# Kernel optimization log

Hardware: AMD Instinct MI355X
Metric: run time of the kernel (lower is better)

## Reference

```python
import jax, jax.numpy as jnp
import numpy as np

# per-item cutpoint counts (from np.unique(item_positions, return_counts=True))
NUM_CUTS = np.array([4, 5, 6, 7] * 4)  # 16 items
N_ITEMS = len(NUM_CUTS)
MAX_CP = int(NUM_CUTS.max())  # 7
CP = jnp.asarray(NUM_CUTS)  # [I]
CUT_MASK = jnp.arange(MAX_CP)[None, :] < CP[:, None]  # [I, MAX_CP] valid cutpoints
EPS = 1e-8

B, D_IN, H1, H2 = 65536, 512, 1024, 512


def setup_inputs() -> dict:
    key = jax.random.key(0)
    ks = jax.random.split(key, 10)
    x = jax.random.normal(ks[0], (B, D_IN), dtype=jnp.float32)
    data = jax.random.randint(ks[1], (B, N_ITEMS), 0, 4, dtype=jnp.int64 if jax.config.jax_enable_x64 else jnp.int32)
    W1 = jax.random.normal(ks[2], (D_IN, H1), dtype=jnp.float32) / np.sqrt(D_IN)
    b1 = jnp.zeros((H1,), jnp.float32)
    W2 = jax.random.normal(ks[3], (H1, H2), dtype=jnp.float32) / np.sqrt(H1)
    b2 = jnp.zeros((H2,), jnp.float32)
    Wf = jax.random.normal(ks[4], (H2, N_ITEMS), dtype=jnp.float32) / np.sqrt(H2)
    bf = jnp.zeros((N_ITEMS,), jnp.float32)
    # ragged per-item cutpoint heads padded to MAX_CP (masked in reference)
    Wk = jax.random.normal(ks[5], (N_ITEMS, H2, MAX_CP), dtype=jnp.float32) / np.sqrt(H2)
    bk = jnp.zeros((N_ITEMS, MAX_CP), jnp.float32)
    return {"x": x, "data": data, "W1": W1, "b1": b1, "W2": W2, "b2": b2,
            "Wf": Wf, "bf": bf, "Wk": Wk, "bk": bk}


def reference(x, data, W1, b1, W2, b2, Wf, bf, Wk, bk):
    # trunk MLP: Linear -> ReLU, twice
    h = jax.nn.relu(x @ W1 + b1)
    h = jax.nn.relu(h @ W2 + b2)  # [B, H2]
    f_x = h @ Wf + bf  # [B, I]
    # batched ragged per-item cutpoint heads (padded GEMM + mask)
    cut = jnp.einsum('bh,ihc->bic', h, Wk) + bk  # [B, I, MAX_CP]
    e = jnp.where(CUT_MASK[None], jnp.clip(jnp.exp(cut), EPS, None), 0.0)
    cum = jnp.cumsum(e, axis=-1)  # monotone cutpoints; pads contribute 0
    cum_probs = jnp.clip(jax.nn.sigmoid(cum - f_x[:, :, None]), EPS, 1.0 - EPS)
    # category probs: [cum0, diffs..., 1 - cum_last], ragged lengths cp_i + 1
    diff = jnp.concatenate([cum_probs[..., :1], cum_probs[..., 1:] - cum_probs[..., :-1]], axis=-1)
    last_cum = cum_probs[:, jnp.arange(N_ITEMS), CP - 1]  # [B, I]
    diff_pad = jnp.pad(diff, ((0, 0), (0, 0), (0, 1)))  # [B, I, MAX_CP+1]
    cat = jnp.arange(MAX_CP + 1)[None, None, :]
    probs = jnp.where(cat < CP[None, :, None], diff_pad,
                      jnp.where(cat == CP[None, :, None], (1.0 - last_cum)[:, :, None], 1.0))
    probs = jnp.clip(probs, EPS, 1.0 - EPS)  # [B, I, MAX_CP+1]
    # NLL: gather observed category per (respondent, item)
    gathered = jnp.take_along_axis(probs, data[:, :, None].astype(jnp.int32), axis=2)[..., 0]
    rec_loss = -jnp.log(gathered).mean(axis=0).sum()
    return rec_loss, probs
```

## Files before the change

### kernel.cpp

```cpp
#include <hip/hip_runtime.h>
#include <cmath>

#define EPSV 1e-8f

typedef __bf16 bf16_t;
typedef __bf16 bf16x8 __attribute__((ext_vector_type(8)));
typedef __bf16 bf16x4 __attribute__((ext_vector_type(4)));
typedef float f32x4 __attribute__((ext_vector_type(4)));

__device__ __forceinline__ void gload16(const void* g, void* l) {
    __builtin_amdgcn_global_load_lds(
        (const __attribute__((address_space(1))) void*)g,
        (__attribute__((address_space(3))) void*)l, 16, 0, 0);
}

__device__ __forceinline__ void qmap(int q, int& row, int& u) {
    int prow = q >> 3;
    int v = (q & 7) ^ (prow & 7);
    row = (prow << 1) | (v >> 2);
    u = v & 3;
}
__device__ __forceinline__ int lds_elem(int row, int u) {
    int prow = row >> 1;
    int v = ((row & 1) << 2) | u;
    return prow * 64 + ((v ^ (prow & 7)) << 3);
}

template<bool RELU>
__global__ __launch_bounds__(512, 2) void gemm256(
    const bf16_t* __restrict__ A, const bf16_t* __restrict__ BT,
    const float* __restrict__ bias, bf16_t* __restrict__ C,
    int N, int K, int nbx)
{
    __shared__ bf16_t sm[2][2][2][8192];

    const int t    = threadIdx.x;
    const int lane = t & 63;
    const int w    = t >> 6;
    const int wr   = w >> 2;
    const int wc   = w & 3;
    const int r16  = lane & 15;
    const int u16  = lane >> 4;

    const int nwg = gridDim.x;
    int bid = blockIdx.x;
    int swz = ((nwg & 7) == 0) ? ((bid & 7) * (nwg >> 3) + (bid >> 3)) : bid;
    const int bx = swz % nbx, by = swz / nbx;
    const int m0 = by << 8, n0 = bx << 8;

    int r0, u0, r1, u1;
    qmap(t, r0, u0);
    qmap(t + 512, r1, u1);
    const bf16_t* gA0 = A  + (size_t)(m0 + r0) * K + (u0 << 3);
    const bf16_t* gA1 = A  + (size_t)(m0 + r1) * K + (u1 << 3);
    const bf16_t* gB0 = BT + (size_t)(n0 + r0) * K + (u0 << 3);
    const bf16_t* gB1 = BT + (size_t)(n0 + r1) * K + (u1 << 3);

    auto STAGE = [&](const bf16_t* g0, const bf16_t* g1, bf16_t* sl, int koff) {
        gload16(g0 + koff, sl + (w << 9));
        gload16(g1 + koff, sl + 4096 + (w << 9));
    };

    int aoff[8], boff[4];
#pragma unroll
    for (int i = 0; i < 8; ++i) aoff[i] = lds_elem((wr << 7) + (i << 4) + r16, u16);
#pragma unroll
    for (int j = 0; j < 4; ++j) boff[j] = lds_elem((wc << 6) + (j << 4) + r16, u16);

    f32x4 acc[8][4];
#pragma unroll
    for (int i = 0; i < 8; ++i)
#pragma unroll
        for (int j = 0; j < 4; ++j) acc[i][j] = (f32x4){0.f, 0.f, 0.f, 0.f};

    const int NT = K >> 6;

    STAGE(gA0, gA1, &sm[0][0][0][0], 0);
    STAGE(gB0, gB1, &sm[0][1][0][0], 0);
    STAGE(gA0, gA1, &sm[0][0][1][0], 32);
    STAGE(gB0, gB1, &sm[0][1][1][0], 32);
    STAGE(gA0, gA1, &sm[1][0][0][0], 64);
    STAGE(gB0, gB1, &sm[1][1][0][0], 64);
    asm volatile("s_waitcnt vmcnt(8)" ::: "memory");
    __builtin_amdgcn_s_barrier();

    for (int kt = 0; kt < NT; ++kt) {
        const int c  = kt & 1;
        const int c1 = c ^ 1;
        const bool s12 = (kt + 1) < NT;
        const bool s34 = (kt + 2) < NT;
        const int k12 = ((kt + 1) << 6) + 32;
        const int k34 = (kt + 2) << 6;
        const bf16_t* sA0 = &sm[c][0][0][0];
        const bf16_t* sA1 = &sm[c][0][1][0];
        const bf16_t* sB0 = &sm[c][1][0][0];
        const bf16_t* sB1 = &sm[c][1][1][0];

        bf16x8 af[4], bfr[4];

#pragma unroll
        for (int j = 0; j < 4; ++j) bfr[j] = *(const bf16x8*)(sB0 + boff[j]);
#pragma unroll
        for (int i = 0; i < 4; ++i) af[i] = *(const bf16x8*)(sA0 + aoff[i]);
        if (s12) STAGE(gA0, gA1, &sm[c1][0][1][0], k12);
        __builtin_amdgcn_s_barrier();
        __builtin_amdgcn_s_setprio(1);
#pragma unroll
        for (int i = 0; i < 4; ++i)
#pragma unroll
            for (int j = 0; j < 4; ++j)
                acc[i][j] = __builtin_amdgcn_mfma_f32_16x16x32_bf16(bfr[j], af[i], acc[i][j], 0, 0, 0);
        __builtin_amdgcn_s_setprio(0);
        __builtin_amdgcn_s_barrier();

#pragma unroll
        for (int i = 0; i < 4; ++i) af[i] = *(const bf16x8*)(sA0 + aoff[4 + i]);
        if (s12) STAGE(gB0, gB1, &sm[c1][1][1][0], k12);
        if (s12) asm volatile("s_waitcnt vmcnt(8)" ::: "memory");
        else     asm volatile("s_waitcnt vmcnt(0)" ::: "memory");
        __builtin_amdgcn_s_barrier();
        __builtin_amdgcn_s_setprio(1);
#pragma unroll
        for (int i = 0; i < 4; ++i)
#pragma unroll
            for (int j = 0; j < 4; ++j)
                acc[4 + i][j] = __builtin_amdgcn_mfma_f32_16x16x32_bf16(bfr[j], af[i], acc[4 + i][j], 0, 0, 0);
        __builtin_amdgcn_s_setprio(0);
        __builtin_amdgcn_s_barrier();

#pragma unroll
        for (int j = 0; j < 4; ++j) bfr[j] = *(const bf16x8*)(sB1 + boff[j]);
#pragma unroll
        for (int i = 0; i < 4; ++i) af[i] = *(const bf16x8*)(sA1 + aoff[i]);
        if (s34) STAGE(gA0, gA1, &sm[c][0][0][0], k34);
        __builtin_amdgcn_s_barrier();
        __builtin_amdgcn_s_setprio(1);
#pragma unroll
        for (int i = 0; i < 4; ++i)
#pragma unroll
            for (int j = 0; j < 4; ++j)
                acc[i][j] = __builtin_amdgcn_mfma_f32_16x16x32_bf16(bfr[j], af[i], acc[i][j], 0, 0, 0);
        __builtin_amdgcn_s_setprio(0);
        __builtin_amdgcn_s_barrier();

#pragma unroll
        for (int i = 0; i < 4; ++i) af[i] = *(const bf16x8*)(sA1 + aoff[4 + i]);
        if (s34) STAGE(gB0, gB1, &sm[c][1][0][0], k34);
        if (s34)      asm volatile("s_waitcnt vmcnt(8)" ::: "memory");
        else if (s12) asm volatile("s_waitcnt vmcnt(4)" ::: "memory");
        __builtin_amdgcn_s_barrier();
        __builtin_amdgcn_s_setprio(1);
#pragma unroll
        for (int i = 0; i < 4; ++i)
#pragma unroll
            for (int j = 0; j < 4; ++j)
                acc[4 + i][j] = __builtin_amdgcn_mfma_f32_16x16x32_bf16(bfr[j], af[i], acc[4 + i][j], 0, 0, 0);
        __builtin_amdgcn_s_setprio(0);
        __builtin_amdgcn_s_barrier();
    }

    __syncthreads();

    char* eb = (char*)&sm[0][0][0][0];
    const int mBb = (wr << 7) + r16;
    const int nBb = (wc << 6) + (u16 << 2);
#pragma unroll
    for (int i = 0; i < 8; ++i) {
        const int m = mBb + (i << 4);
        const int xm = (m & 15) << 4;
#pragma unroll
        for (int j = 0; j < 4; ++j) {
            const int nl = nBb + (j << 4);
            f32x4 bv = *(const f32x4*)(bias + n0 + nl);
            bf16x4 pk;
#pragma unroll
            for (int r = 0; r < 4; ++r) {
                float v = acc[i][j][r] + bv[r];
                if (RELU) v = fmaxf(v, 0.f);
                pk[r] = (bf16_t)v;
            }
            *(bf16x4*)(eb + m * 512 + ((nl << 1) ^ xm)) = pk;
        }
    }
    __syncthreads();
    const int cc = t & 31;
    const int rr = t >> 5;
#pragma unroll
    for (int rp = 0; rp < 16; ++rp) {
        const int m = (rp << 4) + rr;
        bf16x8 v = *(const bf16x8*)(eb + m * 512 + (((cc << 4) ^ ((m & 15) << 4)) & 511));
        *(bf16x8*)(C + (size_t)(m0 + m) * N + n0 + (cc << 3)) = v;
    }
}

#define BM 128
#define BN 128
#define BK 32

template<bool RELU, typename OutT>
__global__ __launch_bounds__(256) void gemm_bf16(
    const bf16_t* __restrict__ A, const bf16_t* __restrict__ BT,
    const float* __restrict__ bias, OutT* __restrict__ C,
    int N, int K)
{
    __shared__ __align__(16) bf16_t As[BM * BK];
    __shared__ __align__(16) bf16_t Bs[BN * BK];

    const int t    = threadIdx.x;
    const int lane = t & 63;
    const int w    = t >> 6;
    const int wm   = (w >> 1) << 6;
    const int wn   = (w & 1) << 6;
    const int m0   = blockIdx.y * BM;
    const int n0   = blockIdx.x * BN;

    const int srow  = t >> 2;
    const int skoff = (t & 3) << 3;

    const bf16_t* Ap = A  + (size_t)(m0 + srow) * K + skoff;
    const bf16_t* Bp = BT + (size_t)(n0 + srow) * K + skoff;
    const size_t rstep = (size_t)64 * K;

    bf16_t* lA0 = As + ((w << 6)      ) * 8;
    bf16_t* lA1 = As + ((w << 6) + 256) * 8;
    bf16_t* lB0 = Bs + ((w << 6)      ) * 8;
    bf16_t* lB1 = Bs + ((w << 6) + 256) * 8;

    f32x4 acc[4][4];
#pragma unroll
    for (int i = 0; i < 4; ++i)
#pragma unroll
        for (int j = 0; j < 4; ++j) acc[i][j] = (f32x4){0.f, 0.f, 0.f, 0.f};

    const int r16  = lane & 15;
    const int kblk = (lane >> 4) << 3;

    for (int k0 = 0; k0 < K; k0 += BK) {
        __syncthreads();
        gload16(Ap + k0,         lA0);
        gload16(Ap + rstep + k0, lA1);
        gload16(Bp + k0,         lB0);
        gload16(Bp + rstep + k0, lB1);
        __syncthreads();

        bf16x8 af[4], bfr[4];
#pragma unroll
        for (int i = 0; i < 4; ++i) {
            af[i]  = *(const bf16x8*)&As[(wm + (i << 4) + r16) * BK + kblk];
            bfr[i] = *(const bf16x8*)&Bs[(wn + (i << 4) + r16) * BK + kblk];
        }
#pragma unroll
        for (int i = 0; i < 4; ++i)
#pragma unroll
            for (int j = 0; j < 4; ++j)
                acc[i][j] = __builtin_amdgcn_mfma_f32_16x16x32_bf16(af[i], bfr[j], acc[i][j], 0, 0, 0);
    }

#pragma unroll
    for (int j = 0; j < 4; ++j) {
        const int col = n0 + wn + (j << 4) + r16;
        const float bv = bias[col];
#pragma unroll
        for (int i = 0; i < 4; ++i) {
            const int rb = m0 + wm + (i << 4) + ((lane >> 4) << 2);
#pragma unroll
            for (int r = 0; r < 4; ++r) {
                float v = acc[i][j][r] + bv;
                if (RELU) v = fmaxf(v, 0.f);
                C[(size_t)(rb + r) * N + col] = (OutT)v;
            }
        }
    }
}

__global__ __launch_bounds__(256) void convert_x(
    const float* __restrict__ in, bf16_t* __restrict__ out, int n8)
{
    int i = blockIdx.x * 256 + threadIdx.x;
    if (i >= n8) return;
    const float4* p = (const float4*)in;
    float4 a = p[2 * i], b = p[2 * i + 1];
    bf16x8 v;
    v[0] = (bf16_t)a.x; v[1] = (bf16_t)a.y; v[2] = (bf16_t)a.z; v[3] = (bf16_t)a.w;
    v[4] = (bf16_t)b.x; v[5] = (bf16_t)b.y; v[6] = (bf16_t)b.z; v[7] = (bf16_t)b.w;
    ((bf16x8*)out)[i] = v;
}

__global__ __launch_bounds__(256) void transpose_w(
    const float* __restrict__ in, bf16_t* __restrict__ out,
    int kshift, int N, int total)
{
    int idx = blockIdx.x * 256 + threadIdx.x;
    if (idx >= total) return;
    int n = idx >> kshift;
    int k = idx & ((1 << kshift) - 1);
    out[idx] = (bf16_t)in[(size_t)k * N + n];
}

__global__ __launch_bounds__(256) void pack_head(
    const float* __restrict__ Wf, const float* __restrict__ bfv,
    const float* __restrict__ Wk, const float* __restrict__ bk,
    bf16_t* __restrict__ WhT, float* __restrict__ bhead)
{
    int idx = blockIdx.x * 256 + threadIdx.x;
    int n = idx >> 9;
    int k = idx & 511;
    float v;
    if (n < 16) {
        v = Wf[k * 16 + n];
    } else {
        int m = n - 16;
        int i = m / 7, c = m % 7;
        v = Wk[(size_t)i * 3584 + (size_t)k * 7 + c];
    }
    WhT[idx] = (bf16_t)v;
    if (idx < 128) bhead[idx] = (idx < 16) ? bfv[idx] : bk[idx - 16];
}

__global__ __launch_bounds__(256) void head_epilogue(
    const float* __restrict__ hd, const int* __restrict__ data,
    float* __restrict__ probs_out, float* __restrict__ partials,
    int row0)
{
    const int t    = threadIdx.x;
    const int lrow = (blockIdx.x << 4) + (t >> 4);
    const int item = t & 15;
    const size_t grow = (size_t)row0 + lrow;
    const float* h = hd + (size_t)lrow * 128;

    const float f  = h[item];
    const int   cp = 4 + (item & 3);

    float cumP[7];
    float cum = 0.f;
#pragma unroll
    for (int c = 0; c < 7; ++c) {
        if (c < cp) {
            float e = fmaxf(expf(h[16 + item * 7 + c]), EPSV);
            cum += e;
            float s = 1.f / (1.f + expf(f - cum));
            cumP[c] = fminf(fmaxf(s, EPSV), 1.f - EPSV);
        } else {
            cumP[c] = 0.f;
        }
    }

    float probs[8];
#pragma unroll
    for (int k = 0; k < 8; ++k) {
        float v;
        if (k < cp) {
            v = (k == 0) ? cumP[0] : (cumP[k] - cumP[k - 1]);
        } else if (k == cp) {
            v = 1.f - cumP[cp - 1];
        } else {
            v = 1.f;
        }
        probs[k] = fminf(fmaxf(v, EPSV), 1.f - EPSV);
    }

    float* dst = probs_out + (grow * 16 + item) * 8;
#pragma unroll
    for (int k = 0; k < 8; ++k) dst[k] = probs[k];

    int d = data[grow * 16 + item];
    float g = probs[0];
#pragma unroll
    for (int k = 1; k < 8; ++k) g = (d == k) ? probs[k] : g;
    float loss = -logf(g);

    __shared__ float red[256];
    red[t] = loss;
    __syncthreads();
#pragma unroll
    for (int s2 = 128; s2 > 0; s2 >>= 1) {
        if (t < s2) red[t] += red[t + s2];
        __syncthreads();
    }
    if (t == 0) partials[(row0 >> 4) + blockIdx.x] = red[0];
}

__global__ __launch_bounds__(256) void reduce_loss(
    const float* __restrict__ partials, int n, float* __restrict__ out, float scale)
{
    __shared__ float red[256];
    float s = 0.f;
    for (int i = threadIdx.x; i < n; i += 256) s += partials[i];
    red[threadIdx.x] = s;
    __syncthreads();
    for (int k = 128; k > 0; k >>= 1) {
        if (threadIdx.x < k) red[threadIdx.x] += red[threadIdx.x + k];
        __syncthreads();
    }
    if (threadIdx.x == 0) out[0] = red[0] * scale;
}

extern "C" void kernel_launch(void* const* d_in, const int* in_sizes, int n_in,
                              void* d_out, int out_size, void* d_ws, size_t ws_size,
                              hipStream_t stream)
{
    const float* x   = (const float*)d_in[0];
    const int*   dat = (const int*)d_in[1];
    const float* W1  = (const float*)d_in[2];
    const float* b1  = (const float*)d_in[3];
    const float* W2  = (const float*)d_in[4];
    const float* b2  = (const float*)d_in[5];
    const float* Wf  = (const float*)d_in[6];
    const float* bfv = (const float*)d_in[7];
    const float* Wk  = (const float*)d_in[8];
    const float* bk  = (const float*)d_in[9];
    float* out = (float*)d_out;

    const int B = 65536, DIN = 512, H1 = 1024, H2 = 512;

    char* cur = (char*)d_ws;
    auto carve = [&](size_t bytes) {
        char* p = cur;
        cur += (bytes + 255) & ~(size_t)255;
        return p;
    };
    float*  partials = (float*)carve(4096 * 4);
    float*  bhead    = (float*)carve(512);
    bf16_t* W1T      = (bf16_t*)carve((size_t)H1 * DIN * 2);
    bf16_t* W2T      = (bf16_t*)carve((size_t)H2 * H1 * 2);
    bf16_t* WhT      = (bf16_t*)carve((size_t)128 * H2 * 2);

    size_t used = (size_t)(cur - (char*)d_ws);
    size_t avail = (ws_size > used + 1024) ? (ws_size - used - 1024) : 0;
    int SLICE = 2048;
    const int cands[6] = {65536, 32768, 16384, 8192, 4096, 2048};
    for (int ci = 0; ci < 6; ++ci) {
        if ((size_t)cands[ci] * 4608 <= avail) { SLICE = cands[ci]; break; }
    }
    bf16_t* xb = (bf16_t*)carve((size_t)SLICE * DIN * 2);
    bf16_t* h1 = (bf16_t*)carve((size_t)SLICE * H1 * 2);
    bf16_t* h2 = (bf16_t*)carve((size_t)SLICE * H2 * 2);
    float*  hd = (float*)carve((size_t)SLICE * 128 * 4);

    transpose_w<<<(H1 * DIN + 255) / 256, 256, 0, stream>>>(W1, W1T, 9,  H1, H1 * DIN);
    transpose_w<<<(H2 * H1 + 255) / 256, 256, 0, stream>>>(W2, W2T, 10, H2, H2 * H1);
    pack_head<<<256, 256, 0, stream>>>(Wf, bfv, Wk, bk, WhT, bhead);

    for (int r0 = 0; r0 < B; r0 += SLICE) {
        convert_x<<<SLICE / 4, 256, 0, stream>>>(x + (size_t)r0 * DIN, xb, SLICE * DIN / 8);
        gemm256<true><<<(SLICE / 256) * (H1 / 256), 512, 0, stream>>>(xb, W1T, b1, h1, H1, DIN, H1 / 256);
        gemm256<true><<<(SLICE / 256) * (H2 / 256), 512, 0, stream>>>(h1, W2T, b2, h2, H2, H1, H2 / 256);
        gemm_bf16<false, float><<<dim3(1, SLICE / 128), 256, 0, stream>>>(h2, WhT, bhead, hd, 128, H2);
        head_epilogue<<<SLICE / 16, 256, 0, stream>>>(hd, dat, out + 1, partials, r0);
    }
    reduce_loss<<<1, 256, 0, stream>>>(partials, B / 16, out, 1.0f / B);
}
```

Measured before the change: 258.4 us.

## Fuse head GEMM with ordinal epilogue and prefetch A fragments in gemm256

The head GEMM and the cutpoint/probability epilogue become one kernel. The 128x128 fp32 head outputs stay in LDS instead of being written to and re-read from a global buffer, which removes one launch per slice and the round trip through HBM. Separately, the main GEMM main loop now double-buffers A fragments in registers, loading the next sub-tile's A right after a barrier so LDS reads overlap the MFMAs. The changes cost more registers and 64KB of LDS per head block, which lowers occupancy of the head kernel.

Result: faster. 237.5 us (-8.1%).

```diff
diff --git a/kernel.cpp b/kernel.cpp
--- a/kernel.cpp
+++ b/kernel.cpp
@@ -83,6 +83,10 @@
     STAGE(gB0, gB1, &sm[1][1][0][0], 64);
     asm volatile("s_waitcnt vmcnt(8)" ::: "memory");
     __builtin_amdgcn_s_barrier();
+
+    bf16x8 af0[4], af1[4], bfr[4];
+#pragma unroll
+    for (int i = 0; i < 4; ++i) af0[i] = *(const bf16x8*)(&sm[0][0][0][0] + aoff[i]);
 
     for (int kt = 0; kt < NT; ++kt) {
         const int c  = kt & 1;
@@ -96,12 +100,10 @@
         const bf16_t* sB0 = &sm[c][1][0][0];
         const bf16_t* sB1 = &sm[c][1][1][0];
 
-        bf16x8 af[4], bfr[4];
-
 #pragma unroll
         for (int j = 0; j < 4; ++j) bfr[j] = *(const bf16x8*)(sB0 + boff[j]);
 #pragma unroll
-        for (int i = 0; i < 4; ++i) af[i] = *(const bf16x8*)(sA0 + aoff[i]);
+        for (int i = 0; i < 4; ++i) af1[i] = *(const bf16x8*)(sA0 + aoff[4 + i]);
         if (s12) STAGE(gA0, gA1, &sm[c1][0][1][0], k12);
         __builtin_amdgcn_s_barrier();
         __builtin_amdgcn_s_setprio(1);
@@ -109,29 +111,29 @@
         for (int i = 0; i < 4; ++i)
 #pragma unroll
             for (int j = 0; j < 4; ++j)
-                acc[i][j] = __builtin_amdgcn_mfma_f32_16x16x32_bf16(bfr[j], af[i], acc[i][j], 0, 0, 0);
+                acc[i][j] = __builtin_amdgcn_mfma_f32_16x16x32_bf16(bfr[j], af0[i], acc[i][j], 0, 0, 0);
         __builtin_amdgcn_s_setprio(0);
         __builtin_amdgcn_s_barrier();
 
-#pragma unroll
-        for (int i = 0; i < 4; ++i) af[i] = *(const bf16x8*)(sA0 + aoff[4 + i]);
         if (s12) STAGE(gB0, gB1, &sm[c1][1][1][0], k12);
         if (s12) asm volatile("s_waitcnt vmcnt(8)" ::: "memory");
         else     asm volatile("s_waitcnt vmcnt(0)" ::: "memory");
         __builtin_amdgcn_s_barrier();
+#pragma unroll
+        for (int i = 0; i < 4; ++i) af0[i] = *(const bf16x8*)(sA1 + aoff[i]);
         __builtin_amdgcn_s_setprio(1);
 #pragma unroll
         for (int i = 0; i < 4; ++i)
 #pragma unroll
             for (int j = 0; j < 4; ++j)
-                acc[4 + i][j] = __builtin_amdgcn_mfma_f32_16x16x32_bf16(bfr[j], af[i], acc[4 + i][j], 0, 0, 0);
+                acc[4 + i][j] = __builtin_amdgcn_mfma_f32_16x16x32_bf16(bfr[j], af1[i], acc[4 + i][j], 0, 0, 0);
         __builtin_amdgcn_s_setprio(0);
         __builtin_amdgcn_s_barrier();
 
 #pragma unroll
         for (int j = 0; j < 4; ++j) bfr[j] = *(const bf16x8*)(sB1 + boff[j]);
 #pragma unroll
-        for (int i = 0; i < 4; ++i) af[i] = *(const bf16x8*)(sA1 + aoff[i]);
+        for (int i = 0; i < 4; ++i) af1[i] = *(const bf16x8*)(sA1 + aoff[4 + i]);
         if (s34) STAGE(gA0, gA1, &sm[c][0][0][0], k34);
         __builtin_amdgcn_s_barrier();
         __builtin_amdgcn_s_setprio(1);
@@ -139,22 +141,25 @@
         for (int i = 0; i < 4; ++i)
 #pragma unroll
             for (int j = 0; j < 4; ++j)
-                acc[i][j] = __builtin_amdgcn_mfma_f32_16x16x32_bf16(bfr[j], af[i], acc[i][j], 0, 0, 0);
+                acc[i][j] = __builtin_amdgcn_mfma_f32_16x16x32_bf16(bfr[j], af0[i], acc[i][j], 0, 0, 0);
         __builtin_amdgcn_s_setprio(0);
         __builtin_amdgcn_s_barrier();
 
-#pragma unroll
-        for (int i = 0; i < 4; ++i) af[i] = *(const bf16x8*)(sA1 + aoff[4 + i]);
         if (s34) STAGE(gB0, gB1, &sm[c][1][0][0], k34);
         if (s34)      asm volatile("s_waitcnt vmcnt(8)" ::: "memory");
         else if (s12) asm volatile("s_waitcnt vmcnt(4)" ::: "memory");
         __builtin_amdgcn_s_barrier();
+        if (s12) {
+#pragma unroll
+            for (int i = 0; i < 4; ++i)
+                af0[i] = *(const bf16x8*)(&sm[c1][0][0][0] + aoff[i]);
+        }
         __builtin_amdgcn_s_setprio(1);
 #pragma unroll
         for (int i = 0; i < 4; ++i)
 #pragma unroll
             for (int j = 0; j < 4; ++j)
-                acc[4 + i][j] = __builtin_amdgcn_mfma_f32_16x16x32_bf16(bfr[j], af[i], acc[4 + i][j], 0, 0, 0);
+                acc[4 + i][j] = __builtin_amdgcn_mfma_f32_16x16x32_bf16(bfr[j], af1[i], acc[4 + i][j], 0, 0, 0);
         __builtin_amdgcn_s_setprio(0);
         __builtin_amdgcn_s_barrier();
     }
@@ -193,32 +198,28 @@
     }
 }
 
-#define BM 128
-#define BN 128
-#define BK 32
-
-template<bool RELU, typename OutT>
-__global__ __launch_bounds__(256) void gemm_bf16(
+__global__ __launch_bounds__(256) void head_fused(
     const bf16_t* __restrict__ A, const bf16_t* __restrict__ BT,
-    const float* __restrict__ bias, OutT* __restrict__ C,
-    int N, int K)
-{
-    __shared__ __align__(16) bf16_t As[BM * BK];
-    __shared__ __align__(16) bf16_t Bs[BN * BK];
+    const float* __restrict__ bias, const int* __restrict__ data,
+    float* __restrict__ probs_out, float* __restrict__ partials,
+    int K, int row0)
+{
+    __shared__ __align__(16) bf16_t As[128 * 32];
+    __shared__ __align__(16) bf16_t Bs[128 * 32];
+    __shared__ float hdl[128 * 128];
 
     const int t    = threadIdx.x;
     const int lane = t & 63;
     const int w    = t >> 6;
     const int wm   = (w >> 1) << 6;
     const int wn   = (w & 1) << 6;
-    const int m0   = blockIdx.y * BM;
-    const int n0   = blockIdx.x * BN;
+    const int m0l  = blockIdx.x << 7;
 
     const int srow  = t >> 2;
     const int skoff = (t & 3) << 3;
 
-    const bf16_t* Ap = A  + (size_t)(m0 + srow) * K + skoff;
-    const bf16_t* Bp = BT + (size_t)(n0 + srow) * K + skoff;
+    const bf16_t* Ap = A  + (size_t)(m0l + srow) * K + skoff;
+    const bf16_t* Bp = BT + (size_t)srow * K + skoff;
     const size_t rstep = (size_t)64 * K;
 
     bf16_t* lA0 = As + ((w << 6)      ) * 8;
@@ -233,9 +234,10 @@
         for (int j = 0; j < 4; ++j) acc[i][j] = (f32x4){0.f, 0.f, 0.f, 0.f};
 
     const int r16  = lane & 15;
-    const int kblk = (lane >> 4) << 3;
-
-    for (int k0 = 0; k0 < K; k0 += BK) {
+    const int u16  = lane >> 4;
+    const int kblk = u16 << 3;
+
+    for (int k0 = 0; k0 < K; k0 += 32) {
         __syncthreads();
         gload16(Ap + k0,         lA0);
         gload16(Ap + rstep + k0, lA1);
@@ -246,8 +248,8 @@
         bf16x8 af[4], bfr[4];
 #pragma unroll
         for (int i = 0; i < 4; ++i) {
-            af[i]  = *(const bf16x8*)&As[(wm + (i << 4) + r16) * BK + kblk];
-            bfr[i] = *(const bf16x8*)&Bs[(wn + (i << 4) + r16) * BK + kblk];
+            af[i]  = *(const bf16x8*)&As[(wm + (i << 4) + r16) * 32 + kblk];
+            bfr[i] = *(const bf16x8*)&Bs[(wn + (i << 4) + r16) * 32 + kblk];
         }
 #pragma unroll
         for (int i = 0; i < 4; ++i)
@@ -258,19 +260,71 @@
 
 #pragma unroll
     for (int j = 0; j < 4; ++j) {
-        const int col = n0 + wn + (j << 4) + r16;
+        const int col = wn + (j << 4) + r16;
         const float bv = bias[col];
 #pragma unroll
         for (int i = 0; i < 4; ++i) {
-            const int rb = m0 + wm + (i << 4) + ((lane >> 4) << 2);
-#pragma unroll
-            for (int r = 0; r < 4; ++r) {
-                float v = acc[i][j][r] + bv;
-                if (RELU) v = fmaxf(v, 0.f);
-                C[(size_t)(rb + r) * N + col] = (OutT)v;
+            const int rb = wm + (i << 4) + (u16 << 2);
+#pragma unroll
+            for (int r = 0; r < 4; ++r)
+                hdl[(rb + r) * 128 + col] = acc[i][j][r] + bv;
+        }
+    }
+    __syncthreads();
+
+    float lsum = 0.f;
+    const int item = t & 15;
+    const int cp   = 4 + (item & 3);
+#pragma unroll
+    for (int p = 0; p < 8; ++p) {
+        const int row = (p << 4) + (t >> 4);
+        const float* h = hdl + row * 128;
+        const size_t grow = (size_t)row0 + m0l + row;
+
+        const float f = h[item];
+        float cumP[7];
+        float cum = 0.f;
+#pragma unroll
+        for (int c = 0; c < 7; ++c) {
+            if (c < cp) {
+                float e = fmaxf(expf(h[16 + item * 7 + c]), EPSV);
+                cum += e;
+                float s = 1.f / (1.f + expf(f - cum));
+                cumP[c] = fminf(fmaxf(s, EPSV), 1.f - EPSV);
+            } else {
+                cumP[c] = 0.f;
             }
         }
-    }
+        float probs[8];
+#pragma unroll
+        for (int k = 0; k < 8; ++k) {
+            float v;
+            if (k < cp)       v = (k == 0) ? cumP[0] : (cumP[k] - cumP[k - 1]);
+            else if (k == cp) v = 1.f - cumP[cp - 1];
+            else              v = 1.f;
+            probs[k] = fminf(fmaxf(v, EPSV), 1.f - EPSV);
+        }
+        float* dst = probs_out + (grow * 16 + item) * 8;
+#pragma unroll
+        for (int k = 0; k < 8; ++k) dst[k] = probs[k];
+
+        const int d = data[grow * 16 + item];
+        float g = probs[0];
+#pragma unroll
+        for (int k = 1; k < 8; ++k) g = (d == k) ? probs[k] : g;
+        lsum += -logf(g);
+    }
+
+    __syncthreads();
+    float* red = (float*)As;
+    red[t] = lsum;
+    __syncthreads();
+#pragma unroll
+    for (int s2 = 128; s2 > 0; s2 >>= 1) {
+        if (t < s2) red[t] += red[t + s2];
+        __syncthreads();
+    }
+    if (t == 0) partials[(row0 >> 7) + blockIdx.x] = red[0];
 }
 
 __global__ __launch_bounds__(256) void convert_x(
@@ -315,69 +369,6 @@
     }
     WhT[idx] = (bf16_t)v;
     if (idx < 128) bhead[idx] = (idx < 16) ? bfv[idx] : bk[idx - 16];
-}
-
-__global__ __launch_bounds__(256) void head_epilogue(
-    const float* __restrict__ hd, const int* __restrict__ data,
-    float* __restrict__ probs_out, float* __restrict__ partials,
-    int row0)
-{
-    const int t    = threadIdx.x;
-    const int lrow = (blockIdx.x << 4) + (t >> 4);
-    const int item = t & 15;
-    const size_t grow = (size_t)row0 + lrow;
-    const float* h = hd + (size_t)lrow * 128;
-
-    const float f  = h[item];
-    const int   cp = 4 + (item & 3);
-
-    float cumP[7];
-    float cum = 0.f;
-#pragma unroll
-    for (int c = 0; c < 7; ++c) {
-        if (c < cp) {
-            float e = fmaxf(expf(h[16 + item * 7 + c]), EPSV);
-            cum += e;
-            float s = 1.f / (1.f + expf(f - cum));
-            cumP[c] = fminf(fmaxf(s, EPSV), 1.f - EPSV);
-        } else {
-            cumP[c] = 0.f;
-        }
-    }
-
-    float probs[8];
-#pragma unroll
-    for (int k = 0; k < 8; ++k) {
-        float v;
-        if (k < cp) {
-            v = (k == 0) ? cumP[0] : (cumP[k] - cumP[k - 1]);
-        } else if (k == cp) {
-            v = 1.f - cumP[cp - 1];
-        } else {
-            v = 1.f;
-        }
-        probs[k] = fminf(fmaxf(v, EPSV), 1.f - EPSV);
-    }
-
-    float* dst = probs_out + (grow * 16 + item) * 8;
-#pragma unroll
-    for (int k = 0; k < 8; ++k) dst[k] = probs[k];
-
-    int d = data[grow * 16 + item];
-    float g = probs[0];
-#pragma unroll
-    for (int k = 1; k < 8; ++k) g = (d == k) ? probs[k] : g;
-    float loss = -logf(g);
-
-    __shared__ float red[256];
-    red[t] = loss;
-    __syncthreads();
-#pragma unroll
-    for (int s2 = 128; s2 > 0; s2 >>= 1) {
-        if (t < s2) red[t] += red[t + s2];
-        __syncthreads();
-    }
-    if (t == 0) partials[(row0 >> 4) + blockIdx.x] = red[0];
 }
 
 __global__ __launch_bounds__(256) void reduce_loss(
@@ -430,12 +421,11 @@
     int SLICE = 2048;
     const int cands[6] = {65536, 32768, 16384, 8192, 4096, 2048};
     for (int ci = 0; ci < 6; ++ci) {
-        if ((size_t)cands[ci] * 4608 <= avail) { SLICE = cands[ci]; break; }
+        if ((size_t)cands[ci] * 4096 <= avail) { SLICE = cands[ci]; break; }
     }
     bf16_t* xb = (bf16_t*)carve((size_t)SLICE * DIN * 2);
     bf16_t* h1 = (bf16_t*)carve((size_t)SLICE * H1 * 2);
     bf16_t* h2 = (bf16_t*)carve((size_t)SLICE * H2 * 2);
-    float*  hd = (float*)carve((size_t)SLICE * 128 * 4);
 
     transpose_w<<<(H1 * DIN + 255) / 256, 256, 0, stream>>>(W1, W1T, 9,  H1, H1 * DIN);
     transpose_w<<<(H2 * H1 + 255) / 256, 256, 0, stream>>>(W2, W2T, 10, H2, H2 * H1);
@@ -445,8 +435,7 @@
         convert_x<<<SLICE / 4, 256, 0, stream>>>(x + (size_t)r0 * DIN, xb, SLICE * DIN / 8);
         gemm256<true><<<(SLICE / 256) * (H1 / 256), 512, 0, stream>>>(xb, W1T, b1, h1, H1, DIN, H1 / 256);
         gemm256<true><<<(SLICE / 256) * (H2 / 256), 512, 0, stream>>>(h1, W2T, b2, h2, H2, H1, H2 / 256);
-        gemm_bf16<false, float><<<dim3(1, SLICE / 128), 256, 0, stream>>>(h2, WhT, bhead, hd, 128, H2);
-        head_epilogue<<<SLICE / 16, 256, 0, stream>>>(hd, dat, out + 1, partials, r0);
-    }
-    reduce_loss<<<1, 256, 0, stream>>>(partials, B / 16, out, 1.0f / B);
-}
+        head_fused<<<SLICE / 128, 256, 0, stream>>>(h2, WhT, bhead, dat, out + 1, partials, H2, r0);
+    }
+    reduce_loss<<<1, 256, 0, stream>>>(partials, B / 128, out, 1.0f / B);
+}
```
